# Optimization experiments

Hardware: AMD Instinct MI355X
Metric: run time of the kernel (lower is better)

## Reference

```python
import jax, jax.numpy as jnp
import numpy as np

N_NODES = 100000
N_EDGES = 1600000
IN_C, HID_C, OUT_C = 128, 128, 64


def gcn_conv(x, src, dst, ew, W, b, n_nodes):
    """PyG GCNConv: symmetric-normalized aggregation with added self-loops.

    out = D^{-1/2} (A + I) D^{-1/2} (x @ W) + b,  D = deg(A+I)
    """
    h = x @ W  # [N, C_out]
    # degree at target nodes, including self-loop weight of 1
    deg = jax.ops.segment_sum(ew, dst, num_segments=n_nodes) + 1.0  # [N]
    dinv = jnp.where(deg > 0, jax.lax.rsqrt(deg), 0.0)
    norm = dinv[src] * ew * dinv[dst]  # [E]
    # gather-scale-scatter over edges + self-loop term (norm_ii = 1/deg_i)
    agg = jax.ops.segment_sum(h[src] * norm[:, None], dst, num_segments=n_nodes)
    agg = agg + h * (dinv * dinv)[:, None]
    return agg + b


def setup_inputs() -> dict:
    key = jax.random.key(0)
    ks = jax.random.split(key, 7)
    x = jax.random.normal(ks[0], (N_NODES, IN_C), dtype=jnp.float32)
    edge_index = jax.random.randint(ks[1], (2, N_EDGES), 0, N_NODES, dtype=jnp.int32)
    edge_weight = jax.random.uniform(ks[2], (N_EDGES,), dtype=jnp.float32)
    W1 = jax.random.normal(ks[3], (IN_C, HID_C), dtype=jnp.float32) / np.sqrt(IN_C)
    b1 = jnp.zeros((HID_C,), dtype=jnp.float32)
    W2 = jax.random.normal(ks[4], (HID_C, OUT_C), dtype=jnp.float32) / np.sqrt(HID_C)
    b2 = jnp.zeros((OUT_C,), dtype=jnp.float32)
    return {"x": x, "edge_index": edge_index, "edge_weight": edge_weight,
            "W1": W1, "b1": b1, "W2": W2, "b2": b2}


def reference(x, edge_index, edge_weight, W1, b1, W2, b2):
    src, dst = edge_index[0], edge_index[1]
    n = x.shape[0]
    h = gcn_conv(x, src, dst, edge_weight, W1, b1, n)
    h = jax.nn.relu(h)
    out = gcn_conv(h, src, dst, edge_weight, W2, b2, n)
    return out
```

## Files before the change

### kernel.cpp

```cpp
#include <hip/hip_runtime.h>


#define N_NODES 100000
#define CHUNK   2048
#define NBUCK   196
#define BSHIFT  9
#define BNODES  512
#define CAP     10240

typedef __attribute__((ext_vector_type(8))) short bf16x8;
typedef __attribute__((ext_vector_type(4))) float f32x4;

__device__ __forceinline__ unsigned bf16r(float f) {
    unsigned u = __float_as_uint(f);
    return (u + 0x7fffu + ((u >> 16) & 1u)) >> 16;
}
__device__ __forceinline__ float bf_lo(unsigned u) { return __uint_as_float(u << 16); }
__device__ __forceinline__ float bf_hi(unsigned u) { return __uint_as_float(u & 0xffff0000u); }


__global__ __launch_bounds__(256) void prepA1_kernel(
    const int* __restrict__ dst, const float* __restrict__ W1,
    const float* __restrict__ W2, unsigned* __restrict__ Wt1,
    unsigned* __restrict__ Wt2, int* __restrict__ histmat, int E)
{
    __shared__ int hist[256];
    int t = threadIdx.x;
    if (blockIdx.x == 0) {
        for (int f = t; f < 128 * 64; f += 256) {
            int c = f % 128, j = f / 128;
            Wt1[c * 64 + j] = bf16r(W1[(size_t)(2 * j) * 128 + c]) |
                              (bf16r(W1[(size_t)(2 * j + 1) * 128 + c]) << 16);
        }
        return;
    }
    if (blockIdx.x == 1) {
        for (int f = t; f < 64 * 64; f += 256) {
            int c = f % 64, j = f / 64;
            Wt2[c * 64 + j] = bf16r(W2[(size_t)(2 * j) * 64 + c]) |
                              (bf16r(W2[(size_t)(2 * j + 1) * 64 + c]) << 16);
        }
        return;
    }
    int blk = blockIdx.x - 2;
    hist[t] = 0;
    __syncthreads();
    int e0 = blk * CHUNK;
    int nv = min(CHUNK, E - e0);
#pragma unroll
    for (int j = 0; j < CHUNK / 256; ++j) {
        int idx = t + j * 256;
        if (idx < nv) atomicAdd(&hist[dst[e0 + idx] >> BSHIFT], 1);
    }
    __syncthreads();
    histmat[blk * 256 + t] = hist[t];
}


__global__ __launch_bounds__(256) void scanB_kernel(
    int* __restrict__ histmat, int* __restrict__ bucketSize, int NBLK)
{
    __shared__ int sums[256];
    int b = blockIdx.x, t = threadIdx.x;
    const int PER = (NBLK + 255) / 256;
    int loc[8];
    int s = 0;
#pragma unroll 8
    for (int j = 0; j < PER; ++j) {
        int r = t * PER + j;
        int v = (r < NBLK) ? histmat[r * 256 + b] : 0;
        loc[j] = v; s += v;
    }
    sums[t] = s;
    __syncthreads();
    int v = s;
#pragma unroll
    for (int off = 1; off < 256; off <<= 1) {
        int a = (t >= off) ? sums[t - off] : 0;
        __syncthreads();
        sums[t] += a;
        __syncthreads();
    }
    if (t == 255) bucketSize[b] = sums[255];
    int run = sums[t] - v;
#pragma unroll 8
    for (int j = 0; j < PER; ++j) {
        int r = t * PER + j;
        if (r < NBLK) { histmat[r * 256 + b] = run; run += loc[j]; }
    }
}


#define A2G_SMEM 52224

__device__ __forceinline__ void a2_body(
    char* smem, int blk,
    const int* __restrict__ src, const int* __restrict__ dst,
    const float* __restrict__ ew, const int* __restrict__ histmat,
    uint2* __restrict__ csrTmp, int E)
{
    int* hist = (int*)smem;
    int* sc   = hist + 256;
    int* exc  = sc + 256;
    int* lcur = exc + 256;
    int* basel= lcur + 256;
    uint2* ent = (uint2*)(basel + 256);
    unsigned short* bof = (unsigned short*)(ent + CHUNK);

    int t = threadIdx.x;
    hist[t] = 0; lcur[t] = 0;
    basel[t] = histmat[blk * 256 + t];
    __syncthreads();

    int e0 = blk * CHUNK;
    int nv = min(CHUNK, E - e0);
    int dv[CHUNK / 256]; int sv[CHUNK / 256]; unsigned wv[CHUNK / 256];
#pragma unroll
    for (int j = 0; j < CHUNK / 256; ++j) {
        int idx = t + j * 256;
        if (idx < nv) {
            int e = e0 + idx;
            dv[j] = dst[e]; sv[j] = src[e]; wv[j] = __float_as_uint(ew[e]);
            atomicAdd(&hist[dv[j] >> BSHIFT], 1);
        } else dv[j] = -1;
    }
    __syncthreads();
    int hv = hist[t];
    sc[t] = hv;
    __syncthreads();
#pragma unroll
    for (int off = 1; off < 256; off <<= 1) {
        int a = (t >= off) ? sc[t - off] : 0;
        __syncthreads();
        sc[t] += a;
        __syncthreads();
    }
    exc[t] = sc[t] - hv;
    __syncthreads();
#pragma unroll
    for (int j = 0; j < CHUNK / 256; ++j) {
        if (dv[j] >= 0) {
            int b  = dv[j] >> BSHIFT;
            int dl = dv[j] & (BNODES - 1);
            int p  = exc[b] + atomicAdd(&lcur[b], 1);
            ent[p] = make_uint2(((unsigned)dl << 17) | (unsigned)sv[j], wv[j]);
            bof[p] = (unsigned short)b;
        }
    }
    __syncthreads();
#pragma unroll
    for (int j = 0; j < CHUNK / 256; ++j) {
        int i = t + j * 256;
        if (i < nv) {
            int b = bof[i];
            csrTmp[(size_t)b * CAP + basel[b] + (i - exc[b])] = ent[i];
        }
    }
}

__device__ __forceinline__ void gemm1_body(
    char* smem, int blk, const float* __restrict__ Xf,
    const unsigned* __restrict__ Wt, unsigned* __restrict__ Hb, int M)
{
    constexpr int LW = 68, KU = 64;
    unsigned* sA = (unsigned*)smem;
    unsigned* sB = sA + 64 * LW;
    const int t = threadIdx.x;
    const int rbase = blk * 64;

    for (int f = t; f < 128 * 16; f += 256) {
        int c = f >> 4, qd = f & 15;
        *(uint4*)&sB[c * LW + qd * 4] = *(const uint4*)&Wt[c * KU + qd * 4];
    }
    for (int f = t; f < 64 * 32; f += 256) {
        int r = f >> 5, c4 = f & 31;
        int gr = rbase + r;
        float4 v = make_float4(0.f, 0.f, 0.f, 0.f);
        if (gr < M) v = *(const float4*)&Xf[(size_t)gr * 128 + c4 * 4];
        sA[r * LW + c4 * 2]     = bf16r(v.x) | (bf16r(v.y) << 16);
        sA[r * LW + c4 * 2 + 1] = bf16r(v.z) | (bf16r(v.w) << 16);
    }
    __syncthreads();

    const int wave = t >> 6, lane = t & 63;
    const int quad = lane >> 4, lr = lane & 15;
    const int n0 = wave * 32;

    f32x4 acc[4][2];
#pragma unroll
    for (int mi = 0; mi < 4; ++mi)
#pragma unroll
        for (int ni = 0; ni < 2; ++ni)
            acc[mi][ni] = (f32x4){0.f, 0.f, 0.f, 0.f};

#pragma unroll
    for (int ks = 0; ks < 4; ++ks) {
        int ko = ks * 16 + quad * 4;
        bf16x8 b0 = *(const bf16x8*)&sB[(n0 + lr) * LW + ko];
        bf16x8 b1 = *(const bf16x8*)&sB[(n0 + 16 + lr) * LW + ko];
#pragma unroll
        for (int mi = 0; mi < 4; ++mi) {
            bf16x8 a = *(const bf16x8*)&sA[(mi * 16 + lr) * LW + ko];
            acc[mi][0] = __builtin_amdgcn_mfma_f32_16x16x32_bf16(a, b0, acc[mi][0], 0, 0, 0);
            acc[mi][1] = __builtin_amdgcn_mfma_f32_16x16x32_bf16(a, b1, acc[mi][1], 0, 0, 0);
        }
    }
    __syncthreads();

    unsigned short* sO = (unsigned short*)sA;
#pragma unroll
    for (int mi = 0; mi < 4; ++mi)
#pragma unroll
        for (int ni = 0; ni < 2; ++ni)
#pragma unroll
            for (int r = 0; r < 4; ++r)
                sO[(mi * 16 + quad * 4 + r) * (2 * LW) + n0 + ni * 16 + lr] =
                    (unsigned short)bf16r(acc[mi][ni][r]);
    __syncthreads();

    for (int f = t; f < 64 * 64; f += 256) {
        int row = f >> 6, cu = f & 63;
        int gr = rbase + row;
        if (gr < M) Hb[(size_t)gr * 64 + cu] = sA[row * LW + cu];
    }
}

__global__ __launch_bounds__(256) void a2_gemm_kernel(
    const int* __restrict__ src, const int* __restrict__ dst,
    const float* __restrict__ ew, const int* __restrict__ histmat,
    uint2* __restrict__ csrTmp, int E, int NBLK,
    const float* __restrict__ x, const unsigned* __restrict__ Wt1,
    unsigned* __restrict__ h1, int M)
{
    __shared__ __align__(16) char smem[A2G_SMEM];
    if ((int)blockIdx.x < NBLK)
        a2_body(smem, blockIdx.x, src, dst, ew, histmat, csrTmp, E);
    else
        gemm1_body(smem, blockIdx.x - NBLK, x, Wt1, h1, M);
}


__global__ __launch_bounds__(1024) void bucketB_kernel(
    const uint2* __restrict__ csrTmp, const int* __restrict__ bucketSize,
    float* __restrict__ dinv, uint2* __restrict__ nodeinfo,
    uint2* __restrict__ csrF, int N)
{
    __shared__ uint2 ent[CAP];
    __shared__ unsigned long long dc[BNODES];
    __shared__ int scn[BNODES], beg[BNODES], cur[BNODES];
    int b = blockIdx.x, t = threadIdx.x;
    if (t < BNODES) { dc[t] = 0ull; cur[t] = 0; }
    __syncthreads();

    int sz = min(bucketSize[b], CAP);
    const uint2* reg = csrTmp + (size_t)b * CAP;
    for (int i = t; i < sz; i += 1024) {
        uint2 en = reg[i];
        ent[i] = en;
        int dl = (int)(en.x >> 17);
        unsigned fx = (unsigned)__float2uint_rn(__uint_as_float(en.y) * 16777216.0f);
        atomicAdd(&dc[dl], (1ull << 32) | (unsigned long long)fx);
    }
    __syncthreads();

    int cnt = 0; float dv = 1.0f;
    if (t < BNODES) {
        unsigned long long v = dc[t];
        cnt = (int)(v >> 32);
        dv = rsqrtf((float)(unsigned)(v & 0xffffffffull) * (1.0f / 16777216.0f) + 1.0f);
        scn[t] = cnt;
    }
    __syncthreads();
#pragma unroll
    for (int off = 1; off < BNODES; off <<= 1) {
        int a = 0;
        if (t < BNODES && t >= off) a = scn[t - off];
        __syncthreads();
        if (t < BNODES) scn[t] += a;
        __syncthreads();
    }
    if (t < BNODES) {
        int excl = scn[t] - cnt;
        beg[t] = excl;
        int gn = b * BNODES + t;
        if (gn < N) {
            dinv[gn] = dv;
            nodeinfo[gn] = make_uint2((unsigned)(b * CAP + excl), (unsigned)cnt);
        }
    }
    __syncthreads();

    uint2* outreg = csrF + (size_t)b * CAP;
    for (int i = t; i < sz; i += 1024) {
        uint2 en = ent[i];
        int dl = (int)(en.x >> 17);
        int p  = beg[dl] + atomicAdd(&cur[dl], 1);
        outreg[p] = make_uint2(en.x & 0x1FFFFu, en.y);
    }
}


__global__ __launch_bounds__(256) void gg_kernel(
    const uint2* __restrict__ nodeinfo, const uint2* __restrict__ csr,
    const uint4* __restrict__ Hb4,
    const float* __restrict__ dinv, const float* __restrict__ bias,
    const unsigned* __restrict__ Wt2, unsigned* __restrict__ H2, int N)
{
    __shared__ __align__(16) unsigned sG[16 * 68];
    __shared__ __align__(16) float    sO[16 * 68];

    const int t = threadIdx.x, wave = t >> 6, lane = t & 63;
    const int q = lane >> 4, cg = lane & 15;
    const int nb = blockIdx.x * 16;

    for (int i = 0; i < 4; ++i) {
        int m = wave * 4 + i;
        int node = nb + m;
        float di = dinv[node];
        float d0 = (q == 0) ? di : 0.f;
        float acc[8];
        {
            uint4 su = Hb4[(size_t)node * 16 + cg];
            acc[0] = bf_lo(su.x) * d0; acc[1] = bf_hi(su.x) * d0;
            acc[2] = bf_lo(su.y) * d0; acc[3] = bf_hi(su.y) * d0;
            acc[4] = bf_lo(su.z) * d0; acc[5] = bf_hi(su.z) * d0;
            acc[6] = bf_lo(su.w) * d0; acc[7] = bf_hi(su.w) * d0;
        }
        uint2 inf = nodeinfo[node];
        int beg = (int)inf.x, end = beg + (int)inf.y;
        for (int j = beg; j < end; j += 64) {
            int cs = 0; float cw = 0.f;
            if (j + lane < end) {
                uint2 p = csr[j + lane];
                cs = (int)p.x;
                cw = __uint_as_float(p.y) * dinv[cs];
            }
            int mm = end - j; if (mm > 64) mm = 64;
#pragma unroll 4
            for (int k = 0; k < mm; k += 4) {
                int   s = __shfl(cs, k + q);
                float w = __shfl(cw, k + q);
                uint4 u = Hb4[(size_t)s * 16 + cg];
                acc[0] = fmaf(bf_lo(u.x), w, acc[0]); acc[1] = fmaf(bf_hi(u.x), w, acc[1]);
                acc[2] = fmaf(bf_lo(u.y), w, acc[2]); acc[3] = fmaf(bf_hi(u.y), w, acc[3]);
                acc[4] = fmaf(bf_lo(u.z), w, acc[4]); acc[5] = fmaf(bf_hi(u.z), w, acc[5]);
                acc[6] = fmaf(bf_lo(u.w), w, acc[6]); acc[7] = fmaf(bf_hi(u.w), w, acc[7]);
            }
        }
#pragma unroll
        for (int v = 0; v < 8; ++v) {
            acc[v] += __shfl_xor(acc[v], 16);
            acc[v] += __shfl_xor(acc[v], 32);
        }
        if (q == 0) {
            int c = cg * 8;
            uint4 pk;
            pk.x = bf16r(fmaxf(acc[0] * di + bias[c + 0], 0.f)) |
                   (bf16r(fmaxf(acc[1] * di + bias[c + 1], 0.f)) << 16);
            pk.y = bf16r(fmaxf(acc[2] * di + bias[c + 2], 0.f)) |
                   (bf16r(fmaxf(acc[3] * di + bias[c + 3], 0.f)) << 16);
            pk.z = bf16r(fmaxf(acc[4] * di + bias[c + 4], 0.f)) |
                   (bf16r(fmaxf(acc[5] * di + bias[c + 5], 0.f)) << 16);
            pk.w = bf16r(fmaxf(acc[6] * di + bias[c + 6], 0.f)) |
                   (bf16r(fmaxf(acc[7] * di + bias[c + 7], 0.f)) << 16);
            *(uint4*)&sG[m * 68 + cg * 4] = pk;
        }
    }
    __syncthreads();

    {
        const int quad = lane >> 4, lr = lane & 15;
        const int n0 = wave * 16;
        f32x4 accv = (f32x4){0.f, 0.f, 0.f, 0.f};
#pragma unroll
        for (int ks = 0; ks < 4; ++ks) {
            int ko = ks * 16 + quad * 4;
            bf16x8 av = *(const bf16x8*)&sG[lr * 68 + ko];
            bf16x8 bv = *(const bf16x8*)&Wt2[(n0 + lr) * 64 + ko];
            accv = __builtin_amdgcn_mfma_f32_16x16x32_bf16(av, bv, accv, 0, 0, 0);
        }
#pragma unroll
        for (int r = 0; r < 4; ++r)
            sO[(quad * 4 + r) * 68 + n0 + lr] = accv[r];
    }
    __syncthreads();

    for (int f = t; f < 512; f += 256) {
        int row = f >> 5, cu = f & 31;
        unsigned pk = bf16r(sO[row * 68 + 2 * cu]) |
                      (bf16r(sO[row * 68 + 2 * cu + 1]) << 16);
        H2[(size_t)(nb + row) * 32 + cu] = pk;
    }
}


__global__ __launch_bounds__(256) void gather64_kernel(
    const uint2* __restrict__ nodeinfo, const uint2* __restrict__ csr,
    const uint4* __restrict__ Hb4,
    const float* __restrict__ dinv, const float* __restrict__ bias,
    float* __restrict__ OUT, int N)
{
    int node = blockIdx.x * 4 + (threadIdx.x >> 6);
    if (node >= N) return;
    int lane = threadIdx.x & 63;
    int q  = lane >> 3;
    int cg = lane & 7;

    float di = dinv[node];
    float d0 = (q == 0) ? di : 0.f;
    float acc[8];
    {
        uint4 su = Hb4[(size_t)node * 8 + cg];
        acc[0] = bf_lo(su.x) * d0; acc[1] = bf_hi(su.x) * d0;
        acc[2] = bf_lo(su.y) * d0; acc[3] = bf_hi(su.y) * d0;
        acc[4] = bf_lo(su.z) * d0; acc[5] = bf_hi(su.z) * d0;
        acc[6] = bf_lo(su.w) * d0; acc[7] = bf_hi(su.w) * d0;
    }

    uint2 inf = nodeinfo[node];
    int beg = (int)inf.x, end = beg + (int)inf.y;
    for (int j = beg; j < end; j += 64) {
        int cs = 0; float cw = 0.f;
        if (j + lane < end) {
            uint2 p = csr[j + lane];
            cs = (int)p.x;
            cw = __uint_as_float(p.y) * dinv[cs];
        }
        int mm = end - j; if (mm > 64) mm = 64;
#pragma unroll 2
        for (int k = 0; k < mm; k += 8) {
            int   s = __shfl(cs, k + q);
            float w = __shfl(cw, k + q);
            uint4 u = Hb4[(size_t)s * 8 + cg];
            acc[0] = fmaf(bf_lo(u.x), w, acc[0]); acc[1] = fmaf(bf_hi(u.x), w, acc[1]);
            acc[2] = fmaf(bf_lo(u.y), w, acc[2]); acc[3] = fmaf(bf_hi(u.y), w, acc[3]);
            acc[4] = fmaf(bf_lo(u.z), w, acc[4]); acc[5] = fmaf(bf_hi(u.z), w, acc[5]);
            acc[6] = fmaf(bf_lo(u.w), w, acc[6]); acc[7] = fmaf(bf_hi(u.w), w, acc[7]);
        }
    }

#pragma unroll
    for (int v = 0; v < 8; ++v) {
        acc[v] += __shfl_xor(acc[v], 8);
        acc[v] += __shfl_xor(acc[v], 16);
        acc[v] += __shfl_xor(acc[v], 32);
    }

    int c = cg * 8 + q;
    OUT[(size_t)node * 64 + c] = acc[q] * di + bias[c];
}

static inline size_t align_up(size_t x) { return (x + 255) & ~size_t(255); }

extern "C" void kernel_launch(void* const* d_in, const int* in_sizes, int n_in,
                              void* d_out, int out_size, void* d_ws, size_t ws_size,
                              hipStream_t stream)
{
    const float* x  = (const float*)d_in[0];
    const int*   ei = (const int*)d_in[1];
    const float* ew = (const float*)d_in[2];
    const float* W1 = (const float*)d_in[3];
    const float* b1 = (const float*)d_in[4];
    const float* W2 = (const float*)d_in[5];
    const float* b2 = (const float*)d_in[6];
    float* out = (float*)d_out;

    const int N = N_NODES;
    const int E = in_sizes[2];
    const int* src = ei;
    const int* dst = ei + E;

    const int NBLK = (E + CHUNK - 1) / CHUNK;
    const size_t REGION = (size_t)NBUCK * CAP;
    const int GEMM1B = (N + 63) / 64;

    char* ws = (char*)d_ws;
    int*   histmat   = (int*)ws;   ws += align_up((size_t)NBLK * 256 * 4);
    int*   bucketSize= (int*)ws;   ws += align_up((size_t)NBUCK * 4);
    float* dinv      = (float*)ws; ws += align_up((size_t)N * 4);
    uint2* nodeinfo  = (uint2*)ws; ws += align_up((size_t)N * 8);
    uint2* csrTmp    = (uint2*)ws; ws += align_up(REGION * 8);
    uint2* csrF      = (uint2*)ws; ws += align_up(REGION * 8);
    unsigned* Wt1    = (unsigned*)ws; ws += align_up((size_t)128 * 64 * 4);
    unsigned* Wt2    = (unsigned*)ws; ws += align_up((size_t)64 * 64 * 4);
    unsigned* h1     = (unsigned*)ws; ws += align_up((size_t)N * 64 * 4);
    unsigned* h2     = (unsigned*)ws; ws += align_up((size_t)N * 32 * 4);

    prepA1_kernel<<<NBLK + 2, 256, 0, stream>>>(dst, W1, W2, Wt1, Wt2, histmat, E);
    scanB_kernel<<<NBUCK, 256, 0, stream>>>(histmat, bucketSize, NBLK);
    a2_gemm_kernel<<<NBLK + GEMM1B, 256, 0, stream>>>(
        src, dst, ew, histmat, csrTmp, E, NBLK, x, Wt1, h1, N);
    bucketB_kernel<<<NBUCK, 1024, 0, stream>>>(csrTmp, bucketSize, dinv, nodeinfo, csrF, N);
    gg_kernel<<<N / 16, 256, 0, stream>>>(nodeinfo, csrF, (const uint4*)h1,
                                          dinv, b1, Wt2, h2, N);
    gather64_kernel<<<(N + 3) / 4, 256, 0, stream>>>(
        nodeinfo, csrF, (const uint4*)h2, dinv, b2, out, N);
}
```

Baseline: 289.1 us.

## Pre-scale GEMM outputs by source dinv to drop per-edge dinv gathers

Splits the fused a2/gemm1 kernel so gemm1 runs after bucketB and can multiply each row of h1 by dinv before storing it. gg_kernel likewise scales h2 by dinv on output. Both gather kernels then stop loading dinv[src] for every edge, and the self-loop term uses the already-scaled row. gg_kernel also moves to 512 threads with two nodes per wave, and only four waves run the small MFMA. The cost is that the GEMM no longer overlaps the edge-scatter kernel, and h1/h2 are rounded to bf16 after scaling.

```diff
diff --git a/kernel.cpp b/kernel.cpp
--- a/kernel.cpp
+++ b/kernel.cpp
@@ -91,23 +91,16 @@
 }
 
 
-#define A2G_SMEM 52224
-
-__device__ __forceinline__ void a2_body(
-    char* smem, int blk,
+__global__ __launch_bounds__(256) void a2_kernel(
     const int* __restrict__ src, const int* __restrict__ dst,
     const float* __restrict__ ew, const int* __restrict__ histmat,
     uint2* __restrict__ csrTmp, int E)
 {
-    int* hist = (int*)smem;
-    int* sc   = hist + 256;
-    int* exc  = sc + 256;
-    int* lcur = exc + 256;
-    int* basel= lcur + 256;
-    uint2* ent = (uint2*)(basel + 256);
-    unsigned short* bof = (unsigned short*)(ent + CHUNK);
-
-    int t = threadIdx.x;
+    __shared__ int hist[256], sc[256], exc[256], lcur[256], basel[256];
+    __shared__ uint2 ent[CHUNK];
+    __shared__ unsigned short bof[CHUNK];
+
+    int t = threadIdx.x, blk = blockIdx.x;
     hist[t] = 0; lcur[t] = 0;
     basel[t] = histmat[blk * 256 + t];
     __syncthreads();
@@ -156,87 +149,6 @@
             csrTmp[(size_t)b * CAP + basel[b] + (i - exc[b])] = ent[i];
         }
     }
-}
-
-__device__ __forceinline__ void gemm1_body(
-    char* smem, int blk, const float* __restrict__ Xf,
-    const unsigned* __restrict__ Wt, unsigned* __restrict__ Hb, int M)
-{
-    constexpr int LW = 68, KU = 64;
-    unsigned* sA = (unsigned*)smem;
-    unsigned* sB = sA + 64 * LW;
-    const int t = threadIdx.x;
-    const int rbase = blk * 64;
-
-    for (int f = t; f < 128 * 16; f += 256) {
-        int c = f >> 4, qd = f & 15;
-        *(uint4*)&sB[c * LW + qd * 4] = *(const uint4*)&Wt[c * KU + qd * 4];
-    }
-    for (int f = t; f < 64 * 32; f += 256) {
-        int r = f >> 5, c4 = f & 31;
-        int gr = rbase + r;
-        float4 v = make_float4(0.f, 0.f, 0.f, 0.f);
-        if (gr < M) v = *(const float4*)&Xf[(size_t)gr * 128 + c4 * 4];
-        sA[r * LW + c4 * 2]     = bf16r(v.x) | (bf16r(v.y) << 16);
-        sA[r * LW + c4 * 2 + 1] = bf16r(v.z) | (bf16r(v.w) << 16);
-    }
-    __syncthreads();
-
-    const int wave = t >> 6, lane = t & 63;
-    const int quad = lane >> 4, lr = lane & 15;
-    const int n0 = wave * 32;
-
-    f32x4 acc[4][2];
-#pragma unroll
-    for (int mi = 0; mi < 4; ++mi)
-#pragma unroll
-        for (int ni = 0; ni < 2; ++ni)
-            acc[mi][ni] = (f32x4){0.f, 0.f, 0.f, 0.f};
-
-#pragma unroll
-    for (int ks = 0; ks < 4; ++ks) {
-        int ko = ks * 16 + quad * 4;
-        bf16x8 b0 = *(const bf16x8*)&sB[(n0 + lr) * LW + ko];
-        bf16x8 b1 = *(const bf16x8*)&sB[(n0 + 16 + lr) * LW + ko];
-#pragma unroll
-        for (int mi = 0; mi < 4; ++mi) {
-            bf16x8 a = *(const bf16x8*)&sA[(mi * 16 + lr) * LW + ko];
-            acc[mi][0] = __builtin_amdgcn_mfma_f32_16x16x32_bf16(a, b0, acc[mi][0], 0, 0, 0);
-            acc[mi][1] = __builtin_amdgcn_mfma_f32_16x16x32_bf16(a, b1, acc[mi][1], 0, 0, 0);
-        }
-    }
-    __syncthreads();
-
-    unsigned short* sO = (unsigned short*)sA;
-#pragma unroll
-    for (int mi = 0; mi < 4; ++mi)
-#pragma unroll
-        for (int ni = 0; ni < 2; ++ni)
-#pragma unroll
-            for (int r = 0; r < 4; ++r)
-                sO[(mi * 16 + quad * 4 + r) * (2 * LW) + n0 + ni * 16 + lr] =
-                    (unsigned short)bf16r(acc[mi][ni][r]);
-    __syncthreads();
-
-    for (int f = t; f < 64 * 64; f += 256) {
-        int row = f >> 6, cu = f & 63;
-        int gr = rbase + row;
-        if (gr < M) Hb[(size_t)gr * 64 + cu] = sA[row * LW + cu];
-    }
-}
-
-__global__ __launch_bounds__(256) void a2_gemm_kernel(
-    const int* __restrict__ src, const int* __restrict__ dst,
-    const float* __restrict__ ew, const int* __restrict__ histmat,
-    uint2* __restrict__ csrTmp, int E, int NBLK,
-    const float* __restrict__ x, const unsigned* __restrict__ Wt1,
-    unsigned* __restrict__ h1, int M)
-{
-    __shared__ __align__(16) char smem[A2G_SMEM];
-    if ((int)blockIdx.x < NBLK)
-        a2_body(smem, blockIdx.x, src, dst, ew, histmat, csrTmp, E);
-    else
-        gemm1_body(smem, blockIdx.x - NBLK, x, Wt1, h1, M);
 }
 
 
@@ -300,7 +212,79 @@
 }
 
 
-__global__ __launch_bounds__(256) void gg_kernel(
+__global__ __launch_bounds__(256) void gemm1_kernel(
+    const float* __restrict__ Xf, const unsigned* __restrict__ Wt,
+    const float* __restrict__ dinv, unsigned* __restrict__ Hb, int M)
+{
+    constexpr int LW = 68, KU = 64;
+    __shared__ unsigned sA[64 * LW];
+    __shared__ unsigned sB[128 * LW];
+    __shared__ float sD[64];
+    const int t = threadIdx.x;
+    const int rbase = blockIdx.x * 64;
+
+    if (t < 64) sD[t] = (rbase + t < M) ? dinv[rbase + t] : 0.f;
+    for (int f = t; f < 128 * 16; f += 256) {
+        int c = f >> 4, qd = f & 15;
+        *(uint4*)&sB[c * LW + qd * 4] = *(const uint4*)&Wt[c * KU + qd * 4];
+    }
+    for (int f = t; f < 64 * 32; f += 256) {
+        int r = f >> 5, c4 = f & 31;
+        int gr = rbase + r;
+        float4 v = make_float4(0.f, 0.f, 0.f, 0.f);
+        if (gr < M) v = *(const float4*)&Xf[(size_t)gr * 128 + c4 * 4];
+        sA[r * LW + c4 * 2]     = bf16r(v.x) | (bf16r(v.y) << 16);
+        sA[r * LW + c4 * 2 + 1] = bf16r(v.z) | (bf16r(v.w) << 16);
+    }
+    __syncthreads();
+
+    const int wave = t >> 6, lane = t & 63;
+    const int quad = lane >> 4, lr = lane & 15;
+    const int n0 = wave * 32;
+
+    f32x4 acc[4][2];
+#pragma unroll
+    for (int mi = 0; mi < 4; ++mi)
+#pragma unroll
+        for (int ni = 0; ni < 2; ++ni)
+            acc[mi][ni] = (f32x4){0.f, 0.f, 0.f, 0.f};
+
+#pragma unroll
+    for (int ks = 0; ks < 4; ++ks) {
+        int ko = ks * 16 + quad * 4;
+        bf16x8 b0 = *(const bf16x8*)&sB[(n0 + lr) * LW + ko];
+        bf16x8 b1 = *(const bf16x8*)&sB[(n0 + 16 + lr) * LW + ko];
+#pragma unroll
+        for (int mi = 0; mi < 4; ++mi) {
+            bf16x8 a = *(const bf16x8*)&sA[(mi * 16 + lr) * LW + ko];
+            acc[mi][0] = __builtin_amdgcn_mfma_f32_16x16x32_bf16(a, b0, acc[mi][0], 0, 0, 0);
+            acc[mi][1] = __builtin_amdgcn_mfma_f32_16x16x32_bf16(a, b1, acc[mi][1], 0, 0, 0);
+        }
+    }
+    __syncthreads();
+
+    unsigned short* sO = (unsigned short*)sA;
+#pragma unroll
+    for (int mi = 0; mi < 4; ++mi)
+#pragma unroll
+        for (int ni = 0; ni < 2; ++ni)
+#pragma unroll
+            for (int r = 0; r < 4; ++r) {
+                int row = mi * 16 + quad * 4 + r;
+                sO[row * (2 * LW) + n0 + ni * 16 + lr] =
+                    (unsigned short)bf16r(acc[mi][ni][r] * sD[row]);
+            }
+    __syncthreads();
+
+    for (int f = t; f < 64 * 64; f += 256) {
+        int row = f >> 6, cu = f & 63;
+        int gr = rbase + row;
+        if (gr < M) Hb[(size_t)gr * 64 + cu] = sA[row * LW + cu];
+    }
+}
+
+
+__global__ __launch_bounds__(512) void gg_kernel(
     const uint2* __restrict__ nodeinfo, const uint2* __restrict__ csr,
     const uint4* __restrict__ Hb4,
     const float* __restrict__ dinv, const float* __restrict__ bias,
@@ -308,23 +292,24 @@
 {
     __shared__ __align__(16) unsigned sG[16 * 68];
     __shared__ __align__(16) float    sO[16 * 68];
+    __shared__ float sDi[16];
 
     const int t = threadIdx.x, wave = t >> 6, lane = t & 63;
     const int q = lane >> 4, cg = lane & 15;
     const int nb = blockIdx.x * 16;
-
-    for (int i = 0; i < 4; ++i) {
-        int m = wave * 4 + i;
+    if (t < 16) sDi[t] = dinv[nb + t];
+
+    for (int i = 0; i < 2; ++i) {
+        int m = wave * 2 + i;
         int node = nb + m;
-        float di = dinv[node];
-        float d0 = (q == 0) ? di : 0.f;
+        float one0 = (q == 0) ? 1.f : 0.f;
         float acc[8];
         {
             uint4 su = Hb4[(size_t)node * 16 + cg];
-            acc[0] = bf_lo(su.x) * d0; acc[1] = bf_hi(su.x) * d0;
-            acc[2] = bf_lo(su.y) * d0; acc[3] = bf_hi(su.y) * d0;
-            acc[4] = bf_lo(su.z) * d0; acc[5] = bf_hi(su.z) * d0;
-            acc[6] = bf_lo(su.w) * d0; acc[7] = bf_hi(su.w) * d0;
+            acc[0] = bf_lo(su.x) * one0; acc[1] = bf_hi(su.x) * one0;
+            acc[2] = bf_lo(su.y) * one0; acc[3] = bf_hi(su.y) * one0;
+            acc[4] = bf_lo(su.z) * one0; acc[5] = bf_hi(su.z) * one0;
+            acc[6] = bf_lo(su.w) * one0; acc[7] = bf_hi(su.w) * one0;
         }
         uint2 inf = nodeinfo[node];
         int beg = (int)inf.x, end = beg + (int)inf.y;
@@ -333,7 +318,7 @@
             if (j + lane < end) {
                 uint2 p = csr[j + lane];
                 cs = (int)p.x;
-                cw = __uint_as_float(p.y) * dinv[cs];
+                cw = __uint_as_float(p.y);
             }
             int mm = end - j; if (mm > 64) mm = 64;
 #pragma unroll 4
@@ -353,6 +338,7 @@
             acc[v] += __shfl_xor(acc[v], 32);
         }
         if (q == 0) {
+            float di = dinv[node];
             int c = cg * 8;
             uint4 pk;
             pk.x = bf16r(fmaxf(acc[0] * di + bias[c + 0], 0.f)) |
@@ -368,7 +354,7 @@
     }
     __syncthreads();
 
-    {
+    if (wave < 4) {
         const int quad = lane >> 4, lr = lane & 15;
         const int n0 = wave * 16;
         f32x4 accv = (f32x4){0.f, 0.f, 0.f, 0.f};
@@ -385,10 +371,11 @@
     }
     __syncthreads();
 
-    for (int f = t; f < 512; f += 256) {
-        int row = f >> 5, cu = f & 31;
-        unsigned pk = bf16r(sO[row * 68 + 2 * cu]) |
-                      (bf16r(sO[row * 68 + 2 * cu + 1]) << 16);
+    if (t < 512) {
+        int row = t >> 5, cu = t & 31;
+        float sc = sDi[row];
+        unsigned pk = bf16r(sO[row * 68 + 2 * cu] * sc) |
+                      (bf16r(sO[row * 68 + 2 * cu + 1] * sc) << 16);
         H2[(size_t)(nb + row) * 32 + cu] = pk;
     }
 }
@@ -406,15 +393,14 @@
     int q  = lane >> 3;
     int cg = lane & 7;
 
-    float di = dinv[node];
-    float d0 = (q == 0) ? di : 0.f;
+    float one0 = (q == 0) ? 1.f : 0.f;
     float acc[8];
     {
         uint4 su = Hb4[(size_t)node * 8 + cg];
-        acc[0] = bf_lo(su.x) * d0; acc[1] = bf_hi(su.x) * d0;
-        acc[2] = bf_lo(su.y) * d0; acc[3] = bf_hi(su.y) * d0;
-        acc[4] = bf_lo(su.z) * d0; acc[5] = bf_hi(su.z) * d0;
-        acc[6] = bf_lo(su.w) * d0; acc[7] = bf_hi(su.w) * d0;
+        acc[0] = bf_lo(su.x) * one0; acc[1] = bf_hi(su.x) * one0;
+        acc[2] = bf_lo(su.y) * one0; acc[3] = bf_hi(su.y) * one0;
+        acc[4] = bf_lo(su.z) * one0; acc[5] = bf_hi(su.z) * one0;
+        acc[6] = bf_lo(su.w) * one0; acc[7] = bf_hi(su.w) * one0;
     }
 
     uint2 inf = nodeinfo[node];
@@ -424,7 +410,7 @@
         if (j + lane < end) {
             uint2 p = csr[j + lane];
             cs = (int)p.x;
-            cw = __uint_as_float(p.y) * dinv[cs];
+            cw = __uint_as_float(p.y);
         }
         int mm = end - j; if (mm > 64) mm = 64;
 #pragma unroll 2
@@ -447,7 +433,7 @@
     }
 
     int c = cg * 8 + q;
-    OUT[(size_t)node * 64 + c] = acc[q] * di + bias[c];
+    OUT[(size_t)node * 64 + c] = acc[q] * dinv[node] + bias[c];
 }
 
 static inline size_t align_up(size_t x) { return (x + 255) & ~size_t(255); }
@@ -472,7 +458,6 @@
 
     const int NBLK = (E + CHUNK - 1) / CHUNK;
     const size_t REGION = (size_t)NBUCK * CAP;
-    const int GEMM1B = (N + 63) / 64;
 
     char* ws = (char*)d_ws;
     int*   histmat   = (int*)ws;   ws += align_up((size_t)NBLK * 256 * 4);
@@ -488,10 +473,10 @@
 
     prepA1_kernel<<<NBLK + 2, 256, 0, stream>>>(dst, W1, W2, Wt1, Wt2, histmat, E);
     scanB_kernel<<<NBUCK, 256, 0, stream>>>(histmat, bucketSize, NBLK);
-    a2_gemm_kernel<<<NBLK + GEMM1B, 256, 0, stream>>>(
-        src, dst, ew, histmat, csrTmp, E, NBLK, x, Wt1, h1, N);
+    a2_kernel<<<NBLK, 256, 0, stream>>>(src, dst, ew, histmat, csrTmp, E);
     bucketB_kernel<<<NBUCK, 1024, 0, stream>>>(csrTmp, bucketSize, dinv, nodeinfo, csrF, N);
-    gg_kernel<<<N / 16, 256, 0, stream>>>(nodeinfo, csrF, (const uint4*)h1,
+    gemm1_kernel<<<(N + 63) / 64, 256, 0, stream>>>(x, Wt1, dinv, h1, N);
+    gg_kernel<<<N / 16, 512, 0, stream>>>(nodeinfo, csrF, (const uint4*)h1,
                                           dinv, b1, Wt2, h2, N);
     gather64_kernel<<<(N + 3) / 4, 256, 0, stream>>>(
         nodeinfo, csrF, (const uint4*)h2, dinv, b2, out, N);
```

Measured after the change: 282.5 us. 1.02x faster.

## Precompute full symmetric edge norms in CSR build and split bucket kernel

Applied to the files above, without the earlier changes.

The bucket kernel is split into two passes. The first computes degrees, dinv and node offsets. The second scatters edges into the CSR and stores each edge's full normalized weight dinv[src]*ew*dinv[dst], so both gather kernels no longer do a per-edge dinv[src] lookup or the final dinv multiply; the self-loop term uses di*di. The gg kernel also moves from 256 to 1024 threads per block, one node per wave, with only 4 waves doing the MFMA stage. This adds a kernel launch and a second read of csrTmp, plus random dinv reads during the CSR build, in exchange for cheaper gathers in both layers.

```diff
diff --git a/kernel.cpp b/kernel.cpp
--- a/kernel.cpp
+++ b/kernel.cpp
@@ -225,7 +225,7 @@
     }
 }
 
-__global__ __launch_bounds__(256) void a2_gemm_kernel(
+__global__ __launch_bounds__(256) void a2g_kernel(
     const int* __restrict__ src, const int* __restrict__ dst,
     const float* __restrict__ ew, const int* __restrict__ histmat,
     uint2* __restrict__ csrTmp, int E, int NBLK,
@@ -240,23 +240,20 @@
 }
 
 
-__global__ __launch_bounds__(1024) void bucketB_kernel(
+__global__ __launch_bounds__(1024) void b1_kernel(
     const uint2* __restrict__ csrTmp, const int* __restrict__ bucketSize,
-    float* __restrict__ dinv, uint2* __restrict__ nodeinfo,
-    uint2* __restrict__ csrF, int N)
-{
-    __shared__ uint2 ent[CAP];
+    float* __restrict__ dinv, uint2* __restrict__ nodeinfo, int N)
+{
     __shared__ unsigned long long dc[BNODES];
-    __shared__ int scn[BNODES], beg[BNODES], cur[BNODES];
+    __shared__ int scn[BNODES];
     int b = blockIdx.x, t = threadIdx.x;
-    if (t < BNODES) { dc[t] = 0ull; cur[t] = 0; }
+    if (t < BNODES) dc[t] = 0ull;
     __syncthreads();
 
     int sz = min(bucketSize[b], CAP);
     const uint2* reg = csrTmp + (size_t)b * CAP;
     for (int i = t; i < sz; i += 1024) {
         uint2 en = reg[i];
-        ent[i] = en;
         int dl = (int)(en.x >> 17);
         unsigned fx = (unsigned)__float2uint_rn(__uint_as_float(en.y) * 16777216.0f);
         atomicAdd(&dc[dl], (1ull << 32) | (unsigned long long)fx);
@@ -281,26 +278,45 @@
     }
     if (t < BNODES) {
         int excl = scn[t] - cnt;
-        beg[t] = excl;
         int gn = b * BNODES + t;
         if (gn < N) {
             dinv[gn] = dv;
             nodeinfo[gn] = make_uint2((unsigned)(b * CAP + excl), (unsigned)cnt);
         }
     }
-    __syncthreads();
-
-    uint2* outreg = csrF + (size_t)b * CAP;
+}
+
+
+__global__ __launch_bounds__(1024) void b2_kernel(
+    const uint2* __restrict__ csrTmp, const int* __restrict__ bucketSize,
+    const uint2* __restrict__ nodeinfo, const float* __restrict__ dinv,
+    uint2* __restrict__ csrF, int N)
+{
+    __shared__ float dinv_l[BNODES];
+    __shared__ int beg[BNODES], cur[BNODES];
+    int b = blockIdx.x, t = threadIdx.x;
+    if (t < BNODES) {
+        int gn = b * BNODES + t;
+        float dv = 1.0f; int bg = 0;
+        if (gn < N) { uint2 inf = nodeinfo[gn]; bg = (int)inf.x; dv = dinv[gn]; }
+        dinv_l[t] = dv; beg[t] = bg; cur[t] = 0;
+    }
+    __syncthreads();
+
+    int sz = min(bucketSize[b], CAP);
+    const uint2* reg = csrTmp + (size_t)b * CAP;
     for (int i = t; i < sz; i += 1024) {
-        uint2 en = ent[i];
+        uint2 en = reg[i];
         int dl = (int)(en.x >> 17);
+        int s  = (int)(en.x & 0x1FFFFu);
         int p  = beg[dl] + atomicAdd(&cur[dl], 1);
-        outreg[p] = make_uint2(en.x & 0x1FFFFu, en.y);
-    }
-}
-
-
-__global__ __launch_bounds__(256) void gg_kernel(
+        float w = dinv[s] * __uint_as_float(en.y) * dinv_l[dl];
+        csrF[p] = make_uint2((unsigned)s, __float_as_uint(w));
+    }
+}
+
+
+__global__ __launch_bounds__(1024) void gg_kernel(
     const uint2* __restrict__ nodeinfo, const uint2* __restrict__ csr,
     const uint4* __restrict__ Hb4,
     const float* __restrict__ dinv, const float* __restrict__ bias,
@@ -312,19 +328,18 @@
     const int t = threadIdx.x, wave = t >> 6, lane = t & 63;
     const int q = lane >> 4, cg = lane & 15;
     const int nb = blockIdx.x * 16;
-
-    for (int i = 0; i < 4; ++i) {
-        int m = wave * 4 + i;
-        int node = nb + m;
+    const int node = nb + wave;
+
+    {
         float di = dinv[node];
-        float d0 = (q == 0) ? di : 0.f;
+        float w0 = (q == 0) ? di * di : 0.f;
         float acc[8];
         {
             uint4 su = Hb4[(size_t)node * 16 + cg];
-            acc[0] = bf_lo(su.x) * d0; acc[1] = bf_hi(su.x) * d0;
-            acc[2] = bf_lo(su.y) * d0; acc[3] = bf_hi(su.y) * d0;
-            acc[4] = bf_lo(su.z) * d0; acc[5] = bf_hi(su.z) * d0;
-            acc[6] = bf_lo(su.w) * d0; acc[7] = bf_hi(su.w) * d0;
+            acc[0] = bf_lo(su.x) * w0; acc[1] = bf_hi(su.x) * w0;
+            acc[2] = bf_lo(su.y) * w0; acc[3] = bf_hi(su.y) * w0;
+            acc[4] = bf_lo(su.z) * w0; acc[5] = bf_hi(su.z) * w0;
+            acc[6] = bf_lo(su.w) * w0; acc[7] = bf_hi(su.w) * w0;
         }
         uint2 inf = nodeinfo[node];
         int beg = (int)inf.x, end = beg + (int)inf.y;
@@ -333,7 +348,7 @@
             if (j + lane < end) {
                 uint2 p = csr[j + lane];
                 cs = (int)p.x;
-                cw = __uint_as_float(p.y) * dinv[cs];
+                cw = __uint_as_float(p.y);
             }
             int mm = end - j; if (mm > 64) mm = 64;
 #pragma unroll 4
@@ -355,20 +370,20 @@
         if (q == 0) {
             int c = cg * 8;
             uint4 pk;
-            pk.x = bf16r(fmaxf(acc[0] * di + bias[c + 0], 0.f)) |
-                   (bf16r(fmaxf(acc[1] * di + bias[c + 1], 0.f)) << 16);
-            pk.y = bf16r(fmaxf(acc[2] * di + bias[c + 2], 0.f)) |
-                   (bf16r(fmaxf(acc[3] * di + bias[c + 3], 0.f)) << 16);
-            pk.z = bf16r(fmaxf(acc[4] * di + bias[c + 4], 0.f)) |
-                   (bf16r(fmaxf(acc[5] * di + bias[c + 5], 0.f)) << 16);
-            pk.w = bf16r(fmaxf(acc[6] * di + bias[c + 6], 0.f)) |
-                   (bf16r(fmaxf(acc[7] * di + bias[c + 7], 0.f)) << 16);
-            *(uint4*)&sG[m * 68 + cg * 4] = pk;
-        }
-    }
-    __syncthreads();
-
-    {
+            pk.x = bf16r(fmaxf(acc[0] + bias[c + 0], 0.f)) |
+                   (bf16r(fmaxf(acc[1] + bias[c + 1], 0.f)) << 16);
+            pk.y = bf16r(fmaxf(acc[2] + bias[c + 2], 0.f)) |
+                   (bf16r(fmaxf(acc[3] + bias[c + 3], 0.f)) << 16);
+            pk.z = bf16r(fmaxf(acc[4] + bias[c + 4], 0.f)) |
+                   (bf16r(fmaxf(acc[5] + bias[c + 5], 0.f)) << 16);
+            pk.w = bf16r(fmaxf(acc[6] + bias[c + 6], 0.f)) |
+                   (bf16r(fmaxf(acc[7] + bias[c + 7], 0.f)) << 16);
+            *(uint4*)&sG[wave * 68 + cg * 4] = pk;
+        }
+    }
+    __syncthreads();
+
+    if (wave < 4) {
         const int quad = lane >> 4, lr = lane & 15;
         const int n0 = wave * 16;
         f32x4 accv = (f32x4){0.f, 0.f, 0.f, 0.f};
@@ -385,8 +400,8 @@
     }
     __syncthreads();
 
-    for (int f = t; f < 512; f += 256) {
-        int row = f >> 5, cu = f & 31;
+    if (t < 512) {
+        int row = t >> 5, cu = t & 31;
         unsigned pk = bf16r(sO[row * 68 + 2 * cu]) |
                       (bf16r(sO[row * 68 + 2 * cu + 1]) << 16);
         H2[(size_t)(nb + row) * 32 + cu] = pk;
@@ -407,14 +422,14 @@
     int cg = lane & 7;
 
     float di = dinv[node];
-    float d0 = (q == 0) ? di : 0.f;
+    float w0 = (q == 0) ? di * di : 0.f;
     float acc[8];
     {
         uint4 su = Hb4[(size_t)node * 8 + cg];
-        acc[0] = bf_lo(su.x) * d0; acc[1] = bf_hi(su.x) * d0;
-        acc[2] = bf_lo(su.y) * d0; acc[3] = bf_hi(su.y) * d0;
-        acc[4] = bf_lo(su.z) * d0; acc[5] = bf_hi(su.z) * d0;
-        acc[6] = bf_lo(su.w) * d0; acc[7] = bf_hi(su.w) * d0;
+        acc[0] = bf_lo(su.x) * w0; acc[1] = bf_hi(su.x) * w0;
+        acc[2] = bf_lo(su.y) * w0; acc[3] = bf_hi(su.y) * w0;
+        acc[4] = bf_lo(su.z) * w0; acc[5] = bf_hi(su.z) * w0;
+        acc[6] = bf_lo(su.w) * w0; acc[7] = bf_hi(su.w) * w0;
     }
 
     uint2 inf = nodeinfo[node];
@@ -424,7 +439,7 @@
         if (j + lane < end) {
             uint2 p = csr[j + lane];
             cs = (int)p.x;
-            cw = __uint_as_float(p.y) * dinv[cs];
+            cw = __uint_as_float(p.y);
         }
         int mm = end - j; if (mm > 64) mm = 64;
 #pragma unroll 2
@@ -447,7 +462,7 @@
     }
 
     int c = cg * 8 + q;
-    OUT[(size_t)node * 64 + c] = acc[q] * di + bias[c];
+    OUT[(size_t)node * 64 + c] = acc[q] + bias[c];
 }
 
 static inline size_t align_up(size_t x) { return (x + 255) & ~size_t(255); }
@@ -488,11 +503,12 @@
 
     prepA1_kernel<<<NBLK + 2, 256, 0, stream>>>(dst, W1, W2, Wt1, Wt2, histmat, E);
     scanB_kernel<<<NBUCK, 256, 0, stream>>>(histmat, bucketSize, NBLK);
-    a2_gemm_kernel<<<NBLK + GEMM1B, 256, 0, stream>>>(
+    a2g_kernel<<<NBLK + GEMM1B, 256, 0, stream>>>(
         src, dst, ew, histmat, csrTmp, E, NBLK, x, Wt1, h1, N);
-    bucketB_kernel<<<NBUCK, 1024, 0, stream>>>(csrTmp, bucketSize, dinv, nodeinfo, csrF, N);
-    gg_kernel<<<N / 16, 256, 0, stream>>>(nodeinfo, csrF, (const uint4*)h1,
-                                          dinv, b1, Wt2, h2, N);
+    b1_kernel<<<NBUCK, 1024, 0, stream>>>(csrTmp, bucketSize, dinv, nodeinfo, N);
+    b2_kernel<<<NBUCK, 1024, 0, stream>>>(csrTmp, bucketSize, nodeinfo, dinv, csrF, N);
+    gg_kernel<<<N / 16, 1024, 0, stream>>>(nodeinfo, csrF, (const uint4*)h1,
+                                           dinv, b1, Wt2, h2, N);
     gather64_kernel<<<(N + 3) / 4, 256, 0, stream>>>(
         nodeinfo, csrF, (const uint4*)h2, dinv, b2, out, N);
 }
```

After: 291.8 us. Within noise of the previous version (+0.9%).
